# Optimization experiments

Hardware: AMD Instinct MI355X
Metric: run time of the kernel (lower is better)

Reference implementation:

```python
import jax, jax.numpy as jnp
import numpy as np

B, N, K = 8, 8192, 8192   # batch, out_features, in_features
PACK = 8
# maybe_pack_idxs places original column offset POS[b] into nibble b
POS = [0, 2, 4, 6, 1, 3, 5, 7]
# inverse permutation: original offset p comes from nibble INV[p]
INV = jnp.array([0, 4, 1, 5, 2, 6, 3, 7], dtype=jnp.int32)


def setup_inputs() -> dict:
    key = jax.random.key(0)
    k1, k2 = jax.random.split(key)
    x = jax.random.normal(k1, (B, K), dtype=jnp.float32)
    # random 4-bit codebook indices, then pack exactly like maybe_pack_idxs
    idxs = jax.random.randint(k2, (N, K), 0, 16, dtype=jnp.int32)
    g = idxs.reshape(N, K // PACK, PACK)
    packed = jnp.zeros((N, K // PACK), dtype=jnp.int32)
    for b, p in enumerate(POS):
        packed = packed + (g[..., p] << jnp.int32(4 * b))
    return {"input": x, "Qidxs": packed}


def decompress_weight(Qidxs):
    # Qidxs: [N, K/8] int32 -> W: [N, K] float32
    shifts = (jnp.arange(PACK, dtype=jnp.int32) * 4)
    nibbles = (Qidxs[..., None] >> shifts) & 0xF       # [N, K/8, 8], nibble order
    unpacked = nibbles[..., INV]                        # restore original column order
    # grid = arange(-8, 8) + 0.5  =>  value = idx - 7.5
    return unpacked.reshape(N, K).astype(jnp.float32) - 7.5


def reference(input, Qidxs):
    W = decompress_weight(Qidxs)          # [N, K]
    return input @ W.T                    # [B, N]
```

## Files before the change

### kernel.cpp

```cpp
#include <hip/hip_runtime.h>
#include <hip/hip_fp16.h>
#include <stdint.h>


typedef _Float16 half8 __attribute__((ext_vector_type(8)));
typedef float floatx16 __attribute__((ext_vector_type(16)));

union H2U { unsigned u; __half2 h; };
union V4H8 { uint4 u4; half8 h8; };

__device__ __forceinline__ unsigned unpack_even(unsigned ws, __half2 c1, __half2 c2) {
    H2U t; t.u = (ws & 0x000F000Fu) | 0x64006400u;
    t.h = __hadd2(__hadd2(t.h, c1), c2);
    return t.u;
}
__device__ __forceinline__ unsigned unpack_odd(unsigned ws, __half2 cs, __half2 cc) {
    H2U t; t.u = (ws & 0x00F000F0u) | 0x64006400u;
    t.h = __hfma2(t.h, cs, cc);
    return t.u;
}

#define BPITCH 136
#define BBUF   (32 * BPITCH)
#define APITCH 272
#define ATBL   (16 * APITCH)
#define NW     8
#define AB0    (NW * 2 * BBUF)
#define RED0   (AB0 + NW * 2 * ATBL)
#define LDS_BYTES (RED0 + NW * 1024)

__global__ __launch_bounds__(512, 2)
void hi4b_gemm(const float* __restrict__ x, const int* __restrict__ q,
               float* __restrict__ out)
{
    extern __shared__ char lds[];
    const int tid  = threadIdx.x;
    const int lane = tid & 63;
    const int wv   = tid >> 6;
    const int n0   = blockIdx.x * 32;

    const int nlo = lane & 31;
    const int u   = lane >> 5;
    const int sh  = 8 * u;
    const int c   = lane & 7;
    const int r0  = lane >> 3;

    const uint4*  q4 = (const uint4*)q;
    const float4* x4 = (const float4*)x;

    const int qbase = (n0 + r0) * 256 + wv * 32 + c;
    const int slot = lane & 15, shi = lane >> 4;
    const int uu = slot >> 3, rr = slot & 7;
    const int xbase = rr * 2048 + wv * 256 + uu;

    char* Bw = lds + wv * 2 * BBUF;
    char* T0 = lds + AB0 + wv * 2 * ATBL;
    char* T1 = T0 + ATBL;

    if (lane < 16) {
        *(uint4*)(T0 + lane * APITCH + 256) = make_uint4(0u, 0u, 0u, 0u);
        *(uint4*)(T1 + lane * APITCH + 256) = make_uint4(0u, 0u, 0u, 0u);
    }

    uint4 rb0, rb1, rb2, rb3;
    float4 ra[8];

    auto loadB = [&](int sc) {
        int b = qbase + sc * 8;
        rb0 = q4[b];
        rb1 = q4[b +  8 * 256];
        rb2 = q4[b + 16 * 256];
        rb3 = q4[b + 24 * 256];
    };
    auto writeB = [&](int d) {
        char* Bb = Bw + d * BBUF;
        char* p0 = Bb + (r0     ) * BPITCH + c * 16;
        char* p1 = Bb + (r0 +  8) * BPITCH + c * 16;
        char* p2 = Bb + (r0 + 16) * BPITCH + c * 16;
        char* p3 = Bb + (r0 + 24) * BPITCH + c * 16;
        *(uint2*)(p0)     = make_uint2(rb0.x, rb0.y);
        *(uint2*)(p0 + 8) = make_uint2(rb0.z, rb0.w);
        *(uint2*)(p1)     = make_uint2(rb1.x, rb1.y);
        *(uint2*)(p1 + 8) = make_uint2(rb1.z, rb1.w);
        *(uint2*)(p2)     = make_uint2(rb2.x, rb2.y);
        *(uint2*)(p2 + 8) = make_uint2(rb2.z, rb2.w);
        *(uint2*)(p3)     = make_uint2(rb3.x, rb3.y);
        *(uint2*)(p3 + 8) = make_uint2(rb3.z, rb3.w);
    };
    auto loadA = [&](int sc) {
        #pragma unroll
        for (int i = 0; i < 4; ++i) {
            int s = 4 * i + shi;
            int xi = xbase + sc * 64 + 4 * s;
            ra[2 * i]     = x4[xi];
            ra[2 * i + 1] = x4[xi + 2];
        }
    };
    auto writeA = [&](char* T) {
        #pragma unroll
        for (int i = 0; i < 4; ++i) {
            int s = 4 * i + shi;
            H2U a0, a1, a2, a3;
            a0.h = __floats2half2_rn(ra[2*i].x,   ra[2*i].y);
            a1.h = __floats2half2_rn(ra[2*i].z,   ra[2*i].w);
            a2.h = __floats2half2_rn(ra[2*i+1].x, ra[2*i+1].y);
            a3.h = __floats2half2_rn(ra[2*i+1].z, ra[2*i+1].w);
            *(uint4*)(T + s * APITCH + slot * 16) = make_uint4(a0.u, a1.u, a2.u, a3.u);
        }
    };

    const __half2 c1 = __floats2half2_rn(-1024.0f, -1024.0f);
    const __half2 c2 = __floats2half2_rn(-7.5f, -7.5f);
    const __half2 cs = __floats2half2_rn(0.0625f, 0.0625f);
    const __half2 cc = __floats2half2_rn(-71.5f, -71.5f);

    floatx16 acc;
    #pragma unroll
    for (int i = 0; i < 16; ++i) acc[i] = 0.0f;

    const int aoff = (nlo < 8) ? (u * 8 + nlo) * 16 : 256;
    const char* apL0 = T0 + aoff;
    const char* apL1 = T1 + aoff;

    auto compute = [&](int d, const char* apL) {
        const char* bp = Bw + d * BBUF + nlo * BPITCH;
        #pragma unroll
        for (int s = 0; s < 16; ++s) {
            uint2 w2 = *(const uint2*)(bp + s * 8);
            V4H8 A;  A.u4 = *(const uint4*)(apL + s * APITCH);
            unsigned wsa = w2.x >> sh;
            unsigned wsb = w2.y >> sh;
            V4H8 Bf;
            Bf.u4.x = unpack_even(wsa, c1, c2);
            Bf.u4.y = unpack_odd (wsa, cs, cc);
            Bf.u4.z = unpack_even(wsb, c1, c2);
            Bf.u4.w = unpack_odd (wsb, cs, cc);
            acc = __builtin_amdgcn_mfma_f32_32x32x16_f16(A.h8, Bf.h8, acc, 0, 0, 0);
        }
    };

    loadB(0); loadA(0);
    writeB(0); writeA(T0);
    loadB(1); loadA(1);
    writeB(1); writeA(T1);
    loadB(2); loadA(2);
    compute(0, apL0);
    writeB(0); writeA(T0);
    loadB(3); loadA(3);
    compute(1, apL1);
    writeB(1); writeA(T1);
    compute(0, apL0);
    compute(1, apL1);

    {
        float* red = (float*)(lds + RED0 + wv * 1024);
        #pragma unroll
        for (int r = 0; r < 4; ++r)
            red[(r + 4 * u) * 32 + nlo] = acc[r];
    }
    __syncthreads();
    if (tid < 256) {
        const int b = tid >> 5, nl = tid & 31;
        const float* rd = (const float*)(lds + RED0);
        float sm = 0.0f;
        #pragma unroll
        for (int w = 0; w < NW; ++w)
            sm += rd[w * 256 + b * 32 + nl];
        out[b * 8192 + n0 + nl] = sm;
    }
}

extern "C" void kernel_launch(void* const* d_in, const int* in_sizes, int n_in,
                              void* d_out, int out_size, void* d_ws, size_t ws_size,
                              hipStream_t stream)
{
    const float* x = (const float*)d_in[0];
    const int*   q = (const int*)d_in[1];
    float* out = (float*)d_out;

    hipLaunchKernelGGL(hi4b_gemm, dim3(256), dim3(512), LDS_BYTES, stream,
                       x, q, out);
}
```

Measured before the change: 19.86 us.

## Split K across 16 waves per block with single-buffered per-wave LDS

Doubles the waves per block from 8 to 16 so each wave handles half the K range, two chunks instead of four. The per-wave LDS tile drops from double-buffered to a single buffer, and the reduction area reuses the tile space, which now needs an extra barrier before the reduction. The aim is more memory-level parallelism and shorter per-wave serial chains. The cost is a longer cross-wave reduction and less overlap of loads with compute inside a wave. The launch bounds of 1024 threads and 4 blocks may constrain register allocation.

```diff
diff --git a/kernel.cpp b/kernel.cpp
--- a/kernel.cpp
+++ b/kernel.cpp
@@ -24,12 +24,11 @@
 #define BBUF   (32 * BPITCH)
 #define APITCH 272
 #define ATBL   (16 * APITCH)
-#define NW     8
-#define AB0    (NW * 2 * BBUF)
-#define RED0   (AB0 + NW * 2 * ATBL)
-#define LDS_BYTES (RED0 + NW * 1024)
+#define WLDS   (BBUF + ATBL)
+#define NW     16
+#define LDS_BYTES (NW * WLDS)
 
-__global__ __launch_bounds__(512, 2)
+__global__ __launch_bounds__(1024, 4)
 void hi4b_gemm(const float* __restrict__ x, const int* __restrict__ q,
                float* __restrict__ out)
 {
@@ -48,19 +47,16 @@
     const uint4*  q4 = (const uint4*)q;
     const float4* x4 = (const float4*)x;
 
-    const int qbase = (n0 + r0) * 256 + wv * 32 + c;
+    const int qbase = (n0 + r0) * 256 + wv * 16 + c;
     const int slot = lane & 15, shi = lane >> 4;
     const int uu = slot >> 3, rr = slot & 7;
-    const int xbase = rr * 2048 + wv * 256 + uu;
+    const int xbase = rr * 2048 + wv * 128 + uu;
 
-    char* Bw = lds + wv * 2 * BBUF;
-    char* T0 = lds + AB0 + wv * 2 * ATBL;
-    char* T1 = T0 + ATBL;
+    char* Bw = lds + wv * WLDS;
+    char* Aw = Bw + BBUF;
 
-    if (lane < 16) {
-        *(uint4*)(T0 + lane * APITCH + 256) = make_uint4(0u, 0u, 0u, 0u);
-        *(uint4*)(T1 + lane * APITCH + 256) = make_uint4(0u, 0u, 0u, 0u);
-    }
+    if (lane < 16)
+        *(uint4*)(Aw + lane * APITCH + 256) = make_uint4(0u, 0u, 0u, 0u);
 
     uint4 rb0, rb1, rb2, rb3;
     float4 ra[8];
@@ -72,12 +68,11 @@
         rb2 = q4[b + 16 * 256];
         rb3 = q4[b + 24 * 256];
     };
-    auto writeB = [&](int d) {
-        char* Bb = Bw + d * BBUF;
-        char* p0 = Bb + (r0     ) * BPITCH + c * 16;
-        char* p1 = Bb + (r0 +  8) * BPITCH + c * 16;
-        char* p2 = Bb + (r0 + 16) * BPITCH + c * 16;
-        char* p3 = Bb + (r0 + 24) * BPITCH + c * 16;
+    auto writeB = [&]() {
+        char* p0 = Bw + (r0     ) * BPITCH + c * 16;
+        char* p1 = Bw + (r0 +  8) * BPITCH + c * 16;
+        char* p2 = Bw + (r0 + 16) * BPITCH + c * 16;
+        char* p3 = Bw + (r0 + 24) * BPITCH + c * 16;
         *(uint2*)(p0)     = make_uint2(rb0.x, rb0.y);
         *(uint2*)(p0 + 8) = make_uint2(rb0.z, rb0.w);
         *(uint2*)(p1)     = make_uint2(rb1.x, rb1.y);
@@ -96,7 +91,7 @@
             ra[2 * i + 1] = x4[xi + 2];
         }
     };
-    auto writeA = [&](char* T) {
+    auto writeA = [&]() {
         #pragma unroll
         for (int i = 0; i < 4; ++i) {
             int s = 4 * i + shi;
@@ -105,7 +100,7 @@
             a1.h = __floats2half2_rn(ra[2*i].z,   ra[2*i].w);
             a2.h = __floats2half2_rn(ra[2*i+1].x, ra[2*i+1].y);
             a3.h = __floats2half2_rn(ra[2*i+1].z, ra[2*i+1].w);
-            *(uint4*)(T + s * APITCH + slot * 16) = make_uint4(a0.u, a1.u, a2.u, a3.u);
+            *(uint4*)(Aw + s * APITCH + slot * 16) = make_uint4(a0.u, a1.u, a2.u, a3.u);
         }
     };
 
@@ -119,15 +114,14 @@
     for (int i = 0; i < 16; ++i) acc[i] = 0.0f;
 
     const int aoff = (nlo < 8) ? (u * 8 + nlo) * 16 : 256;
-    const char* apL0 = T0 + aoff;
-    const char* apL1 = T1 + aoff;
+    const char* ap = Aw + aoff;
+    const char* bp = Bw + nlo * BPITCH;
 
-    auto compute = [&](int d, const char* apL) {
-        const char* bp = Bw + d * BBUF + nlo * BPITCH;
+    auto compute = [&]() {
         #pragma unroll
         for (int s = 0; s < 16; ++s) {
             uint2 w2 = *(const uint2*)(bp + s * 8);
-            V4H8 A;  A.u4 = *(const uint4*)(apL + s * APITCH);
+            V4H8 A;  A.u4 = *(const uint4*)(ap + s * APITCH);
             unsigned wsa = w2.x >> sh;
             unsigned wsb = w2.y >> sh;
             V4H8 Bf;
@@ -140,20 +134,15 @@
     };
 
     loadB(0); loadA(0);
-    writeB(0); writeA(T0);
+    writeB(); writeA();
     loadB(1); loadA(1);
-    writeB(1); writeA(T1);
-    loadB(2); loadA(2);
-    compute(0, apL0);
-    writeB(0); writeA(T0);
-    loadB(3); loadA(3);
-    compute(1, apL1);
-    writeB(1); writeA(T1);
-    compute(0, apL0);
-    compute(1, apL1);
+    compute();
+    writeB(); writeA();
+    compute();
 
+    __syncthreads();
     {
-        float* red = (float*)(lds + RED0 + wv * 1024);
+        float* red = (float*)lds + wv * 256;
         #pragma unroll
         for (int r = 0; r < 4; ++r)
             red[(r + 4 * u) * 32 + nlo] = acc[r];
@@ -161,7 +150,7 @@
     __syncthreads();
     if (tid < 256) {
         const int b = tid >> 5, nl = tid & 31;
-        const float* rd = (const float*)(lds + RED0);
+        const float* rd = (const float*)lds;
         float sm = 0.0f;
         #pragma unroll
         for (int w = 0; w < NW; ++w)
@@ -178,6 +167,6 @@
     const int*   q = (const int*)d_in[1];
     float* out = (float*)d_out;
 
-    hipLaunchKernelGGL(hi4b_gemm, dim3(256), dim3(512), LDS_BYTES, stream,
+    hipLaunchKernelGGL(hi4b_gemm, dim3(256), dim3(1024), LDS_BYTES, stream,
                        x, q, out);
 }
```

Result: faster. 16.10 us, median of 2 (-18.9%).
